# Optimization experiments

Measured on AMD Instinct MI355X. Metric: run time of the kernel, lower is better.

Reference implementation:

```python
import jax, jax.numpy as jnp
import numpy as np

D = 64      # in_feats
OUT = 64    # out_feats
MEM = 4     # mem_size
NREL = 8    # num_rels
N = 20000   # num nodes
E = 50000   # num edges
FF = 16     # dim_feedforward (hardcoded in module)
NH = 4      # nhead (hardcoded)
EPS = 1e-5  # LayerNorm eps (torch default)


def _ln(x, w, b):
    m = x.mean(-1, keepdims=True)
    v = ((x - m) ** 2).mean(-1, keepdims=True)
    return (x - m) * jax.lax.rsqrt(v + EPS) * w + b


def _enc(x, Wqkv, bqkv, Wo, bo, W1, b1, W2, b2, ln1w, ln1b, ln2w, ln2b):
    # torch TransformerEncoderLayer, batch_first, post-norm, eval mode, no padding mask (all-zero mask)
    B, S, d = x.shape
    dh = d // NH
    qkv = x @ Wqkv.T + bqkv
    q, k, v = jnp.split(qkv, 3, axis=-1)
    q = q.reshape(B, S, NH, dh)
    k = k.reshape(B, S, NH, dh)
    v = v.reshape(B, S, NH, dh)
    att = jax.nn.softmax(jnp.einsum('bqhd,bkhd->bhqk', q, k) / jnp.sqrt(jnp.float32(dh)), axis=-1)
    o = jnp.einsum('bhqk,bkhd->bqhd', att, v).reshape(B, S, d) @ Wo.T + bo
    x = _ln(x + o, ln1w, ln1b)
    ff = jax.nn.relu(x @ W1.T + b1) @ W2.T + b2
    return _ln(x + ff, ln2w, ln2b)


def setup_inputs() -> dict:
    key = jax.random.key(0)
    ks = jax.random.split(key, 16)
    s = 0.05
    inp = {
        'feat': jax.random.normal(ks[0], (N, D), jnp.float32),
        'src_idx': jax.random.randint(ks[1], (E,), 0, N),
        'dst_idx': jax.random.randint(ks[2], (E,), 0, N),
        'etype': jax.random.randint(ks[3], (E,), 0, NREL),
        'Wqkv': jax.random.normal(ks[4], (3 * D, D), jnp.float32) * s,
        'bqkv': jnp.zeros((3 * D,), jnp.float32),
        'Wo': jax.random.normal(ks[5], (D, D), jnp.float32) * s,
        'bo': jnp.zeros((D,), jnp.float32),
        'W1': jax.random.normal(ks[6], (FF, D), jnp.float32) * s,
        'b1': jnp.zeros((FF,), jnp.float32),
        'W2': jax.random.normal(ks[7], (D, FF), jnp.float32) * s,
        'b2': jnp.zeros((D,), jnp.float32),
        'ln1w': jnp.ones((D,), jnp.float32),
        'ln1b': jnp.zeros((D,), jnp.float32),
        'ln2w': jnp.ones((D,), jnp.float32),
        'ln2b': jnp.zeros((D,), jnp.float32),
        'Wc': jax.random.normal(ks[8], (MEM, D), jnp.float32) * s,
        'bc': jnp.zeros((MEM,), jnp.float32),
        'CLS': jax.random.normal(ks[9], (MEM, D), jnp.float32),
        'SEP': jax.random.normal(ks[10], (D,), jnp.float32),
        'Wm': jax.random.normal(ks[11], (OUT * D, D), jnp.float32) * s,
        'h_bias': jnp.zeros((OUT,), jnp.float32),
    }
    return inp


def reference(feat, src_idx, dst_idx, etype, Wqkv, bqkv, Wo, bo, W1, b1, W2, b2,
              ln1w, ln1b, ln2w, ln2b, Wc, bc, CLS, SEP, Wm, h_bias):
    enc_args = (Wqkv, bqkv, Wo, bo, W1, b1, W2, b2, ln1w, ln1b, ln2w, ln2b)

    def cls_pass(s_, d_):
        # run the shared encoder MEM times with a different CLS token; the math
        # is identical for every relation type, so no per-etype partition needed
        B = s_.shape[0]
        outs = []
        mem = jnp.zeros((B, D), s_.dtype)
        for i in range(MEM):
            cls = jnp.broadcast_to(CLS[i], (B, D))[:, None, :]
            sep = jnp.broadcast_to(SEP, (B, D))[:, None, :]
            seq = jnp.concatenate([cls, s_[:, None, :], sep, d_[:, None, :]], axis=1)  # [B,4,D]
            t = _enc(seq, *enc_args)[:, 0, :]
            outs.append(t)
            mem = mem + t
        return mem, jnp.stack(outs)  # [B,D], [MEM,B,D]

    src = feat[src_idx]  # [E,D]
    dst = feat[dst_idx]
    mem_emb, tmps = cls_pass(src, dst)
    cat_all = tmps @ Wc.T + bc               # [MEM,E,MEM]
    w = (mem_emb @ Wm.T).reshape(E, OUT, D)  # per-edge hypernetwork weight
    msg = jnp.einsum('eoi,ei->eo', w, src)   # [E,OUT]

    # dgl fn.mean aggregation over destination nodes (0 for isolated nodes)
    cnt = jax.ops.segment_sum(jnp.ones((E,), msg.dtype), dst_idx, num_segments=N)
    agg = jax.ops.segment_sum(msg, dst_idx, num_segments=N)
    node_rep = jnp.where(cnt[:, None] > 0, agg / jnp.maximum(cnt, 1.0)[:, None], 0.0)
    node_rep = node_rep + h_bias

    # self loop (same hypernetwork path over every node)
    mem_s, _ = cls_pass(feat, feat)
    hs = (mem_s @ Wm.T).reshape(N, OUT, D)
    node_rep = node_rep + jnp.einsum('noi,ni->no', hs, feat)

    # reconstruct torch concat order of category/label: outer loop etype, inner loop mem idx
    et = etype.astype(jnp.int32)
    counts = jax.ops.segment_sum(jnp.ones((E,), jnp.int32), etype, num_segments=NREL)
    start = jnp.concatenate([jnp.zeros((1,), jnp.int32), jnp.cumsum(counts)[:-1].astype(jnp.int32)])
    order = jnp.argsort(etype, stable=True)
    rank = jnp.zeros((E,), jnp.int32).at[order].set(jnp.arange(E, dtype=jnp.int32) - start[et[order]])
    base = start[et] * MEM + rank                                            # [E]
    pos = base[None, :] + jnp.arange(MEM, dtype=jnp.int32)[:, None] * counts[et][None, :]  # [MEM,E]
    category = jnp.zeros((MEM * E, MEM), cat_all.dtype).at[pos.reshape(-1)].set(cat_all.reshape(-1, MEM))
    label = jnp.zeros((MEM * E,), jnp.int32).at[pos.reshape(-1)].set(
        jnp.repeat(jnp.arange(MEM, dtype=jnp.int32), E))
    return node_rep, label, category
```

## Files before the change

### kernel.cpp

```cpp
#include <hip/hip_runtime.h>
#include <hip/hip_bf16.h>

typedef float f32x4_t __attribute__((ext_vector_type(4)));
typedef short bf16x8_t __attribute__((ext_vector_type(8)));

#define MFMA(a, b, c) __builtin_amdgcn_mfma_f32_16x16x32_bf16(a, b, c, 0, 0, 0)

#define C_Q0   0
#define C_S00  256
#define C_S02  272
#define C_VCLS 288
#define C_VSEP 544

__device__ __forceinline__ short f2bf(float x) {
    return (short)__builtin_bit_cast(unsigned short, __float2bfloat16(x));
}
__device__ __forceinline__ float bf2f(short s) {
    return __builtin_bit_cast(float, ((unsigned)(unsigned short)s) << 16);
}
__device__ __forceinline__ float head_sum16(float v) {
#pragma unroll
    for (int off = 1; off < 16; off <<= 1) v += __shfl_xor(v, off, 64);
    return v;
}

__global__ void k_prep(const float* __restrict__ Wo, const float* __restrict__ Wqkv,
                       const float* __restrict__ W1, const float* __restrict__ W2,
                       const float* __restrict__ Wm, const float* __restrict__ Wc,
                       const float* __restrict__ bqkv,
                       const float* __restrict__ CLS, const float* __restrict__ SEP,
                       const int* __restrict__ etype, const int* __restrict__ dst,
                       short* __restrict__ Bpack, short* __restrict__ WoP,
                       short* __restrict__ WkvP, short* __restrict__ W1P,
                       short* __restrict__ W2P, short* __restrict__ WcP,
                       float* __restrict__ consts,
                       int* __restrict__ hist, int* __restrict__ cnt, int E)
{
    int bx = blockIdx.x;
    if (bx < 136) {
        int tid = bx * 256 + threadIdx.x;
        short tmp[8];
        if (tid < 32768) {
            int u = tid, lane = u & 63, nt = (u >> 6) & 3, kstep = u >> 8;
            int o = nt * 16 + (lane & 15);
            int kb = kstep * 32 + (lane >> 4) * 8;
#pragma unroll
            for (int t = 0; t < 8; t++) { int k = kb + t; tmp[t] = f2bf(Wm[(o * 64 + (k >> 6)) * 64 + (k & 63)]); }
            *(bf16x8_t*)&Bpack[(size_t)u * 8] = *(bf16x8_t*)tmp;
        } else if (tid < 33280) {
            int u = tid - 32768, lane = u & 63, nt = (u >> 6) & 3, kstep = u >> 8;
            int o = nt * 16 + (lane & 15), kb = kstep * 32 + (lane >> 4) * 8;
#pragma unroll
            for (int t = 0; t < 8; t++) tmp[t] = f2bf(Wo[o * 64 + kb + t]);
            *(bf16x8_t*)&WoP[(size_t)u * 8] = *(bf16x8_t*)tmp;
        } else if (tid < 34304) {
            int u = tid - 33280, lane = u & 63, nt = (u >> 6) & 7, kstep = u >> 9;
            int col = nt * 16 + (lane & 15), kb = kstep * 32 + (lane >> 4) * 8;
            int row = 64 + col;
#pragma unroll
            for (int t = 0; t < 8; t++) tmp[t] = f2bf(Wqkv[row * 64 + kb + t]);
            *(bf16x8_t*)&WkvP[(size_t)u * 8] = *(bf16x8_t*)tmp;
        } else if (tid < 34432) {
            int u = tid - 34304, lane = u & 63, kstep = u >> 6;
            int f = lane & 15, kb = kstep * 32 + (lane >> 4) * 8;
#pragma unroll
            for (int t = 0; t < 8; t++) tmp[t] = f2bf(W1[f * 64 + kb + t]);
            *(bf16x8_t*)&W1P[(size_t)u * 8] = *(bf16x8_t*)tmp;
        } else if (tid < 34688) {
            int u = tid - 34432, lane = u & 63, nt = u >> 6;
            int o = nt * 16 + (lane & 15), kb = (lane >> 4) * 8;
#pragma unroll
            for (int t = 0; t < 8; t++) { int k = kb + t; tmp[t] = (k < 16) ? f2bf(W2[o * 16 + k]) : (short)0; }
            *(bf16x8_t*)&W2P[(size_t)u * 8] = *(bf16x8_t*)tmp;
        } else if (tid < 34816) {
            int u = tid - 34688, lane = u & 63, kstep = u >> 6;
            int m = lane & 15, kb = kstep * 32 + (lane >> 4) * 8;
#pragma unroll
            for (int t = 0; t < 8; t++) tmp[t] = (m < 4) ? f2bf(Wc[m * 64 + kb + t]) : (short)0;
            *(bf16x8_t*)&WcP[(size_t)u * 8] = *(bf16x8_t*)tmp;
        }
    } else if (bx == 136) {
        if (threadIdx.x < 64) {
            int lane = threadIdx.x;
            float ksep = bqkv[64 + lane], vsep = bqkv[128 + lane];
            for (int c = 0; c < 64; c++) {
                float sc = SEP[c];
                ksep += Wqkv[(64 + lane) * 64 + c] * sc;
                vsep += Wqkv[(128 + lane) * 64 + c] * sc;
            }
            consts[C_VSEP + lane] = vsep;
            for (int i = 0; i < 4; i++) {
                float q0 = bqkv[lane], kcls = bqkv[64 + lane], vcls = bqkv[128 + lane];
                for (int c = 0; c < 64; c++) {
                    float cc = CLS[i * 64 + c];
                    q0   += Wqkv[lane * 64 + c] * cc;
                    kcls += Wqkv[(64 + lane) * 64 + c] * cc;
                    vcls += Wqkv[(128 + lane) * 64 + c] * cc;
                }
                consts[C_Q0 + i * 64 + lane] = q0;
                consts[C_VCLS + i * 64 + lane] = vcls;
                float p00 = head_sum16(q0 * kcls) * 0.25f;
                float p02 = head_sum16(q0 * ksep) * 0.25f;
                if ((lane & 15) == 0) {
                    consts[C_S00 + i * 4 + (lane >> 4)] = p00;
                    consts[C_S02 + i * 4 + (lane >> 4)] = p02;
                }
            }
        }
    } else {
        __shared__ int h[8];
        int chunk = bx - 137;
        int tid = threadIdx.x;
        if (tid < 8) h[tid] = 0;
        __syncthreads();
        int e = chunk * 256 + tid;
        if (e < E) {
            atomicAdd(&h[etype[e]], 1);
            atomicAdd(&cnt[dst[e]], 1);
        }
        __syncthreads();
        if (tid < 8) hist[chunk * 8 + tid] = h[tid];
    }
}

__global__ void k_scan(const int* __restrict__ hist, int* __restrict__ chunkoff,
                       int* __restrict__ startg, int* __restrict__ countsg, int nch,
                       const float* __restrict__ consts, const float* __restrict__ Wqkv,
                       const float* __restrict__ bqkv,
                       short* __restrict__ WqkP, float* __restrict__ bqk)
{
    int lane = threadIdx.x;
    int g = lane & 7, seg = lane >> 3;
    int per = (nch + 7) / 8;
    int c0 = seg * per, c1 = c0 + per; if (c1 > nch) c1 = nch;
    int sum = 0;
    for (int c = c0; c < c1; c++) sum += hist[c * 8 + g];
    int pre = 0, tot = 0;
#pragma unroll
    for (int s2 = 0; s2 < 8; s2++) {
        int v = __shfl(sum, s2 * 8 + g, 64);
        tot += v;
        if (s2 < seg) pre += v;
    }
    int run = pre;
    for (int c = c0; c < c1; c++) { chunkoff[c * 8 + g] = run; run += hist[c * 8 + g]; }
    if (seg == 0) {
        countsg[g] = tot;
        int sg = 0;
#pragma unroll
        for (int g2 = 0; g2 < 8; g2++) { int v = __shfl(tot, g2, 64); if (g2 < g) sg += v; }
        startg[g] = sg;
    }

    int ih = lane & 15, ii = ih & 3, hh = ih >> 2;
    int lh8 = (lane >> 4) * 8;
    short tmp[8];
#pragma unroll
    for (int kstep = 0; kstep < 2; kstep++) {
#pragma unroll
        for (int t = 0; t < 8; t++) {
            int k = kstep * 32 + lh8 + t;
            float s = 0.f;
            for (int u = 0; u < 16; u++)
                s += consts[C_Q0 + ii * 64 + hh * 16 + u] * Wqkv[(64 + hh * 16 + u) * 64 + k];
            tmp[t] = f2bf(0.25f * s);
        }
        *(bf16x8_t*)&WqkP[(size_t)(kstep * 64 + lane) * 8] = *(bf16x8_t*)tmp;
    }
    if (lane < 16) {
        float s = 0.f;
        for (int u = 0; u < 16; u++)
            s += consts[C_Q0 + ii * 64 + hh * 16 + u] * bqkv[64 + hh * 16 + u];
        bqk[lane] = 0.25f * s;
    }
}

__global__ __launch_bounds__(256) void k_kv(const float* __restrict__ feat,
        const short* __restrict__ WkvP, const short* __restrict__ WqkP,
        const float* __restrict__ bqkv, const float* __restrict__ bqk,
        float* __restrict__ vnode, float* __restrict__ qs, int N)
{
    __shared__ __align__(16) short sA[64 * 72];
    int tid = threadIdx.x, lane = tid & 63, w = tid >> 6;
    int l15 = lane & 15, lh = lane >> 4;
    int base = blockIdx.x * 64;
#pragma unroll
    for (int rr = 0; rr < 16; rr++) {
        int row = w * 16 + rr;
        int n = base + row; n = n < N ? n : N - 1;
        sA[row * 72 + lane] = f2bf(feat[(size_t)n * 64 + lane]);
    }
    __syncthreads();
    const bf16x8_t* bp = (const bf16x8_t*)WkvP;
    bf16x8_t bv0 = bp[(0 * 8 + 4 + w) * 64 + lane];
    bf16x8_t bv1 = bp[(1 * 8 + 4 + w) * 64 + lane];
    bf16x8_t bq0 = ((const bf16x8_t*)WqkP)[lane];
    bf16x8_t bq1 = ((const bf16x8_t*)WqkP)[64 + lane];
    int kof = lh * 8;
    int col = w * 16 + l15;
    float biasv = bqkv[128 + col];
    float bqv = bqk[l15];
#pragma unroll
    for (int rt = 0; rt < 4; rt++) {
        bf16x8_t a0 = *(const bf16x8_t*)&sA[(rt * 16 + l15) * 72 + kof];
        bf16x8_t a1 = *(const bf16x8_t*)&sA[(rt * 16 + l15) * 72 + 32 + kof];
        f32x4_t av = {0.f, 0.f, 0.f, 0.f};
        av = MFMA(a0, bv0, av); av = MFMA(a1, bv1, av);
#pragma unroll
        for (int r = 0; r < 4; r++) {
            int n = base + rt * 16 + lh * 4 + r;
            if (n < N) vnode[(size_t)n * 64 + col] = av[r] + biasv;
        }
        if (w == 0) {
            f32x4_t aq = {0.f, 0.f, 0.f, 0.f};
            aq = MFMA(a0, bq0, aq); aq = MFMA(a1, bq1, aq);
#pragma unroll
            for (int r = 0; r < 4; r++) {
                int n = base + rt * 16 + lh * 4 + r;
                if (n < N) qs[(size_t)n * 16 + l15] = aq[r] + bqv;
            }
        }
    }
}

struct EncW {
    const float* consts; const float* CLS; const float* bo;
    const float* b1; const float* b2;
    const float* ln1w; const float* ln1b; const float* ln2w; const float* ln2b;
    const short* WoP; const short* W1P; const short* W2P; const short* WcP;
    const float* bc;
};

__global__ __launch_bounds__(256) void k_enc(const int* __restrict__ src_idx,
        const int* __restrict__ dst_idx,
        const float* __restrict__ vnode, const float* __restrict__ qs, EncW W,
        float* __restrict__ mem_out, float* __restrict__ cat_out, int E, int M)
{
    __shared__ __align__(16) short sA[64 * 72];
    __shared__ __align__(16) short sF[64 * 40];
    int tid = threadIdx.x, lane = tid & 63, w = tid >> 6;
    int l15 = lane & 15, lh = lane >> 4;
    int base = blockIdx.x * 16;

#pragma unroll
    for (int z = 0; z < 4; z++) {
        int zz = z * 64 + lane;
        sF[(w * 16 + (zz >> 4)) * 40 + 16 + (zz & 15)] = 0;
    }

    float attc[4], esum0[4];
#pragma unroll
    for (int i = 0; i < 4; i++) {
        float e0 = __expf(W.consts[C_S00 + i * 4 + lh]);
        float e2 = __expf(W.consts[C_S02 + i * 4 + lh]);
        attc[i]  = e0 * W.consts[C_VCLS + i * 64 + lane] + e2 * W.consts[C_VSEP + lane];
        esum0[i] = e0 + e2;
    }

#pragma unroll
    for (int el = 0; el < 4; el++) {
        int eloc = w * 4 + el;
        int ge = base + eloc; int gc = ge < M ? ge : M - 1;
        int s, d;
        if (gc < E) { s = src_idx[gc]; d = dst_idx[gc]; }
        else        { s = gc - E; d = s; }
        float vs_ = vnode[(size_t)s * 64 + lane];
        float vd  = vnode[(size_t)d * 64 + lane];
        float4 qh_s = *(const float4*)&qs[(size_t)s * 16 + lh * 4];
        float4 qh_d = *(const float4*)&qs[(size_t)d * 16 + lh * 4];
        float qsv[4] = {qh_s.x, qh_s.y, qh_s.z, qh_s.w};
        float qdv[4] = {qh_d.x, qh_d.y, qh_d.z, qh_d.w};
#pragma unroll
        for (int i = 0; i < 4; i++) {
            float e1 = __expf(qsv[i]), e3 = __expf(qdv[i]);
            float inv = 1.0f / (esum0[i] + e1 + e3);
            float att = (attc[i] + e1 * vs_ + e3 * vd) * inv;
            sA[(eloc * 4 + i) * 72 + lane] = f2bf(att);
        }
    }

    int arow = (w * 16 + l15) * 72;
    int kof = lh * 8;

    const bf16x8_t* bpo = (const bf16x8_t*)W.WoP;
    f32x4_t ac0 = {0.f,0.f,0.f,0.f}, ac1 = ac0, ac2 = ac0, ac3 = ac0;
#pragma unroll
    for (int kstep = 0; kstep < 2; kstep++) {
        bf16x8_t a = *(const bf16x8_t*)&sA[arow + kstep * 32 + kof];
        ac0 = MFMA(a, bpo[(kstep * 4 + 0) * 64 + lane], ac0);
        ac1 = MFMA(a, bpo[(kstep * 4 + 1) * 64 + lane], ac1);
        ac2 = MFMA(a, bpo[(kstep * 4 + 2) * 64 + lane], ac2);
        ac3 = MFMA(a, bpo[(kstep * 4 + 3) * 64 + lane], ac3);
    }

    float x[4][4], y[4][4];
#pragma unroll
    for (int r = 0; r < 4; r++) { x[0][r] = ac0[r]; x[1][r] = ac1[r]; x[2][r] = ac2[r]; x[3][r] = ac3[r]; }
    float lw1[4], lb1[4];
#pragma unroll
    for (int nt = 0; nt < 4; nt++) {
        float b = W.bo[nt * 16 + l15];
        lw1[nt] = W.ln1w[nt * 16 + l15]; lb1[nt] = W.ln1b[nt * 16 + l15];
#pragma unroll
        for (int r = 0; r < 4; r++) x[nt][r] += b + W.CLS[r * 64 + nt * 16 + l15];
    }
#pragma unroll
    for (int r = 0; r < 4; r++) {
        float sm = head_sum16(x[0][r] + x[1][r] + x[2][r] + x[3][r]);
        float mu = sm * 0.015625f;
        float vv = 0.f;
#pragma unroll
        for (int nt = 0; nt < 4; nt++) { float dd = x[nt][r] - mu; vv = fmaf(dd, dd, vv); }
        vv = head_sum16(vv);
        float rs = rsqrtf(vv * 0.015625f + 1e-5f);
#pragma unroll
        for (int nt = 0; nt < 4; nt++) y[nt][r] = (x[nt][r] - mu) * rs * lw1[nt] + lb1[nt];
    }
#pragma unroll
    for (int nt = 0; nt < 4; nt++)
#pragma unroll
        for (int r = 0; r < 4; r++)
            sA[(w * 16 + lh * 4 + r) * 72 + nt * 16 + l15] = f2bf(y[nt][r]);

    const bf16x8_t* bp1 = (const bf16x8_t*)W.W1P;
    f32x4_t fa = {0.f,0.f,0.f,0.f};
#pragma unroll
    for (int kstep = 0; kstep < 2; kstep++) {
        bf16x8_t a = *(const bf16x8_t*)&sA[arow + kstep * 32 + kof];
        fa = MFMA(a, bp1[kstep * 64 + lane], fa);
    }
    float b1v = W.b1[l15];
#pragma unroll
    for (int r = 0; r < 4; r++)
        sF[(w * 16 + lh * 4 + r) * 40 + l15] = f2bf(fmaxf(fa[r] + b1v, 0.f));

    const bf16x8_t* bp2 = (const bf16x8_t*)W.W2P;
    bf16x8_t af = *(const bf16x8_t*)&sF[(w * 16 + l15) * 40 + kof];
    f32x4_t z0 = {0.f,0.f,0.f,0.f}, z1 = z0, z2 = z0, z3 = z0;
    z0 = MFMA(af, bp2[0 * 64 + lane], z0);
    z1 = MFMA(af, bp2[1 * 64 + lane], z1);
    z2 = MFMA(af, bp2[2 * 64 + lane], z2);
    z3 = MFMA(af, bp2[3 * 64 + lane], z3);

    float t[4][4];
#pragma unroll
    for (int r = 0; r < 4; r++) { x[0][r] = z0[r]; x[1][r] = z1[r]; x[2][r] = z2[r]; x[3][r] = z3[r]; }
    float lw2[4], lb2[4];
#pragma unroll
    for (int nt = 0; nt < 4; nt++) {
        float b = W.b2[nt * 16 + l15];
        lw2[nt] = W.ln2w[nt * 16 + l15]; lb2[nt] = W.ln2b[nt * 16 + l15];
#pragma unroll
        for (int r = 0; r < 4; r++) x[nt][r] += b + y[nt][r];
    }
#pragma unroll
    for (int r = 0; r < 4; r++) {
        float sm = head_sum16(x[0][r] + x[1][r] + x[2][r] + x[3][r]);
        float mu = sm * 0.015625f;
        float vv = 0.f;
#pragma unroll
        for (int nt = 0; nt < 4; nt++) { float dd = x[nt][r] - mu; vv = fmaf(dd, dd, vv); }
        vv = head_sum16(vv);
        float rs = rsqrtf(vv * 0.015625f + 1e-5f);
#pragma unroll
        for (int nt = 0; nt < 4; nt++) t[nt][r] = (x[nt][r] - mu) * rs * lw2[nt] + lb2[nt];
    }

    int eloc = w * 4 + lh, ge = base + eloc;

    if (base < E) {
#pragma unroll
        for (int nt = 0; nt < 4; nt++)
#pragma unroll
            for (int r = 0; r < 4; r++)
                sA[(w * 16 + lh * 4 + r) * 72 + nt * 16 + l15] = f2bf(t[nt][r]);
        const bf16x8_t* bpc = (const bf16x8_t*)W.WcP;
        f32x4_t ca = {0.f,0.f,0.f,0.f};
#pragma unroll
        for (int kstep = 0; kstep < 2; kstep++) {
            bf16x8_t a = *(const bf16x8_t*)&sA[arow + kstep * 32 + kof];
            ca = MFMA(a, bpc[kstep * 64 + lane], ca);
        }
        if (l15 < 4 && ge < E) {
            float bcv = W.bc[l15];
#pragma unroll
            for (int r = 0; r < 4; r++)
                cat_out[((size_t)r * E + ge) * 4 + l15] = ca[r] + bcv;
        }
    }

    if (ge < M) {
#pragma unroll
        for (int nt = 0; nt < 4; nt++)
            mem_out[(size_t)ge * 64 + nt * 16 + l15] = t[nt][0] + t[nt][1] + t[nt][2] + t[nt][3];
    }
}

__global__ __launch_bounds__(256, 3) void k_hyper(
        const float* __restrict__ feat, const int* __restrict__ src_idx,
        const int* __restrict__ dst_idx, const float* __restrict__ memall,
        const short* __restrict__ Bpack,
        float* __restrict__ agg, float* __restrict__ selfm, int E, int M)
{
    __shared__ short xsT[64 * 132];
    __shared__ __align__(16) short sB[2][8192];
    int tid = threadIdx.x, lane = tid & 63, w = tid >> 6;
    int l15 = lane & 15, lh = lane >> 4, koff = lh * 8;
    int base = blockIdx.x * 128;

    const bf16x8_t* bp = (const bf16x8_t*)Bpack;

    auto stage = [&](int c, int buf) {
#pragma unroll
        for (int jj = 0; jj < 4; ++jj) {
            int j = w * 4 + jj;
            int il_ic = j >> 3, q = j & 7;
            const short* src = (const short*)(bp + (size_t)(c * 2 + il_ic) * 512
                                              + (q >> 2) * 256 + (q & 3) * 64 + lane);
            short* dst = &sB[buf][j * 512];
            __builtin_amdgcn_global_load_lds(
                (const __attribute__((address_space(1))) void*)src,
                (__attribute__((address_space(3))) void*)dst, 16, 0, 0);
        }
    };

    stage(0, 0);

    for (int rr = 0; rr < 32; ++rr) {
        int row = w * 32 + rr, gr = base + row;
        float xv = 0.f;
        if (gr < M) {
            int xi = gr < E ? src_idx[gr] : gr - E;
            xv = feat[(size_t)xi * 64 + lane];
        }
        xsT[lane * 132 + row] = f2bf(xv);
    }

    bf16x8_t am[2][2];
#pragma unroll
    for (int tt = 0; tt < 2; ++tt) {
        int gr = base + w * 32 + tt * 16 + l15;
        const float* mp = memall + (size_t)(gr < M ? gr : 0) * 64 + koff;
#pragma unroll
        for (int kk = 0; kk < 2; ++kk)
#pragma unroll
            for (int t = 0; t < 8; ++t)
                am[tt][kk][t] = f2bf(mp[kk * 32 + t]);
    }

    f32x4_t out[2][4];
#pragma unroll
    for (int tt = 0; tt < 2; ++tt)
#pragma unroll
        for (int nt = 0; nt < 4; ++nt) out[tt][nt] = (f32x4_t){0.f, 0.f, 0.f, 0.f};
    const f32x4_t ZERO = {0.f, 0.f, 0.f, 0.f};

    int xrow0 = w * 32 + lh * 4;

    int cur = 0;
    for (int c = 0; c < 32; ++c) {
        if (c + 1 < 32) {
            stage(c + 1, cur ^ 1);
            asm volatile("s_waitcnt vmcnt(4)" ::: "memory");
        } else {
            asm volatile("s_waitcnt vmcnt(0)" ::: "memory");
        }
        __builtin_amdgcn_s_barrier();
#pragma unroll
        for (int ic = 0; ic < 2; ++ic) {
            int i = c * 2 + ic;
            unsigned long long xw0 = *(const unsigned long long*)&xsT[i * 132 + xrow0];
            unsigned long long xw1 = *(const unsigned long long*)&xsT[i * 132 + xrow0 + 16];
            float x0[4], x1[4];
            {
                unsigned lo0 = (unsigned)xw0, hi0 = (unsigned)(xw0 >> 32);
                unsigned lo1 = (unsigned)xw1, hi1 = (unsigned)(xw1 >> 32);
                x0[0] = __builtin_bit_cast(float, lo0 << 16);
                x0[1] = __builtin_bit_cast(float, lo0 & 0xffff0000u);
                x0[2] = __builtin_bit_cast(float, hi0 << 16);
                x0[3] = __builtin_bit_cast(float, hi0 & 0xffff0000u);
                x1[0] = __builtin_bit_cast(float, lo1 << 16);
                x1[1] = __builtin_bit_cast(float, lo1 & 0xffff0000u);
                x1[2] = __builtin_bit_cast(float, hi1 << 16);
                x1[3] = __builtin_bit_cast(float, hi1 & 0xffff0000u);
            }
            const bf16x8_t* bfr = (const bf16x8_t*)&sB[cur][ic * 4096];
            f32x4_t P0[4], P1[4];
            __builtin_amdgcn_s_setprio(1);
#pragma unroll
            for (int nt = 0; nt < 4; ++nt) {
                bf16x8_t B0 = bfr[nt * 64 + lane];
                bf16x8_t B1 = bfr[(4 + nt) * 64 + lane];
                P0[nt] = MFMA(am[0][0], B0, ZERO);
                P1[nt] = MFMA(am[1][0], B0, ZERO);
                P0[nt] = MFMA(am[0][1], B1, P0[nt]);
                P1[nt] = MFMA(am[1][1], B1, P1[nt]);
            }
            __builtin_amdgcn_s_setprio(0);
#pragma unroll
            for (int nt = 0; nt < 4; ++nt)
#pragma unroll
                for (int r = 0; r < 4; ++r) {
                    out[0][nt][r] = fmaf(x0[r], P0[nt][r], out[0][nt][r]);
                    out[1][nt][r] = fmaf(x1[r], P1[nt][r], out[1][nt][r]);
                }
        }
        __builtin_amdgcn_s_barrier();
        cur ^= 1;
    }

#pragma unroll
    for (int tt = 0; tt < 2; ++tt) {
        int orow = w * 32 + tt * 16 + lh * 4;
        int di[4];
#pragma unroll
        for (int r = 0; r < 4; ++r) {
            int grow = base + orow + r;
            di[r] = (grow < E) ? dst_idx[grow] : 0;
        }
#pragma unroll
        for (int nt = 0; nt < 4; ++nt) {
            int o = nt * 16 + l15;
#pragma unroll
            for (int r = 0; r < 4; ++r) {
                int grow = base + orow + r;
                if (grow < M) {
                    float v = out[tt][nt][r];
                    if (grow < E) atomicAdd(&agg[(size_t)di[r] * 64 + o], v);
                    else selfm[(size_t)(grow - E) * 64 + o] = v;
                }
            }
        }
    }
}

__global__ __launch_bounds__(256) void k_finsc(
        const float* __restrict__ agg, const int* __restrict__ cnt,
        const float* __restrict__ selfm, const float* __restrict__ h_bias,
        float* __restrict__ outp, int N,
        const int* __restrict__ etype, const float* __restrict__ cat_all,
        const int* __restrict__ chunkoff, const int* __restrict__ startg,
        const int* __restrict__ countsg,
        float* __restrict__ out_label, float* __restrict__ out_cat, int E, int FB)
{
    if ((int)blockIdx.x < FB) {
        int t = blockIdx.x * 256 + threadIdx.x;
        if (t < N * 64) {
            int n = t >> 6, o = t & 63;
            int c = cnt[n];
            float av = (c > 0) ? agg[t] / (float)c : 0.f;
            outp[t] = av + h_bias[o] + selfm[t];
        }
    } else {
        __shared__ int wc[4][8];
        int tid = threadIdx.x, lane = tid & 63, w = tid >> 6;
        int chunk = blockIdx.x - FB;
        int e = chunk * 256 + w * 64 + lane;
        int et = (e < E) ? etype[e] : -1;
        unsigned long long mk[8];
#pragma unroll
        for (int g = 0; g < 8; g++) mk[g] = __ballot(et == g);
        if (lane < 8) wc[w][lane] = (int)__popcll(mk[lane]);
        __syncthreads();
        if (et >= 0) {
            unsigned long long lt = (1ull << lane) - 1ull;
            int myr = chunkoff[chunk * 8 + et] + (int)__popcll(mk[et] & lt);
#pragma unroll
            for (int w2 = 0; w2 < 4; w2++) if (w2 < w) myr += wc[w2][et];
            int sg = startg[et], cg = countsg[et];
            size_t pbase = (size_t)sg * 4 + myr;
#pragma unroll
            for (int i = 0; i < 4; i++) {
                size_t pos = pbase + (size_t)i * cg;
                out_label[pos] = (float)i;
                const float* ca = &cat_all[((size_t)i * E + e) * 4];
                float4 cv = {ca[0], ca[1], ca[2], ca[3]};
                *(float4*)&out_cat[pos * 4] = cv;
            }
        }
    }
}

extern "C" void kernel_launch(void* const* d_in, const int* in_sizes, int n_in,
                              void* d_out, int out_size, void* d_ws, size_t ws_size,
                              hipStream_t stream)
{
    const float* feat    = (const float*)d_in[0];
    const int*   src_idx = (const int*)d_in[1];
    const int*   dst_idx = (const int*)d_in[2];
    const int*   etype   = (const int*)d_in[3];
    const float* Wqkv    = (const float*)d_in[4];
    const float* bqkv    = (const float*)d_in[5];
    const float* Wo      = (const float*)d_in[6];
    const float* bo      = (const float*)d_in[7];
    const float* W1      = (const float*)d_in[8];
    const float* b1      = (const float*)d_in[9];
    const float* W2      = (const float*)d_in[10];
    const float* b2      = (const float*)d_in[11];
    const float* ln1w    = (const float*)d_in[12];
    const float* ln1b    = (const float*)d_in[13];
    const float* ln2w    = (const float*)d_in[14];
    const float* ln2b    = (const float*)d_in[15];
    const float* Wc      = (const float*)d_in[16];
    const float* bc      = (const float*)d_in[17];
    const float* CLS     = (const float*)d_in[18];
    const float* SEP     = (const float*)d_in[19];
    const float* Wm      = (const float*)d_in[20];
    const float* h_bias  = (const float*)d_in[21];

    const int N = in_sizes[0] / 64;
    const int E = in_sizes[1];
    const int M = E + N;
    const int NCH = (E + 255) / 256;
    const int FB = (N * 64 + 255) / 256;

    float* ws = (float*)d_ws;
    size_t off = 0;
    auto alloc = [&](size_t n) { float* p = ws + off; off += (n + 63) & ~(size_t)63; return p; };
    float* qs      = alloc((size_t)N * 16);
    float* vnode   = alloc((size_t)N * 64);
    float* mem_all = alloc((size_t)M * 64);
    float* cat_all = alloc((size_t)E * 16);
    float* agg     = alloc((size_t)N * 64 + N);
    int*   cnt     = (int*)(agg + (size_t)N * 64);
    float* selfm   = alloc((size_t)N * 64);
    float* consts  = alloc(1024);
    short* Bpack   = (short*)alloc(131072);
    short* WoP     = (short*)alloc(2048);
    short* WkvP    = (short*)alloc(4096);
    short* W1P     = (short*)alloc(512);
    short* W2P     = (short*)alloc(1024);
    short* WcP     = (short*)alloc(512);
    short* WqkP    = (short*)alloc(512);
    float* bqk     = alloc(64);
    int*   hist    = (int*)alloc(NCH * 8);
    int*   chunkoff= (int*)alloc(NCH * 8);
    int*   startg  = (int*)alloc(8);
    int*   countsg = (int*)alloc(8);

    float* out_node  = (float*)d_out;
    float* out_label = out_node + (size_t)N * 64;
    float* out_cat   = out_label + (size_t)4 * E;

    hipMemsetAsync(agg, 0, ((size_t)N * 64 + N) * sizeof(float), stream);

    k_prep<<<137 + NCH, 256, 0, stream>>>(Wo, Wqkv, W1, W2, Wm, Wc, bqkv, CLS, SEP,
                                          etype, dst_idx, Bpack, WoP, WkvP, W1P, W2P, WcP,
                                          consts, hist, cnt, E);
    k_scan<<<1, 64, 0, stream>>>(hist, chunkoff, startg, countsg, NCH,
                                 consts, Wqkv, bqkv, WqkP, bqk);

    k_kv<<<(N + 63) / 64, 256, 0, stream>>>(feat, WkvP, WqkP, bqkv, bqk, vnode, qs, N);

    EncW W{consts, CLS, bo, b1, b2, ln1w, ln1b, ln2w, ln2b, WoP, W1P, W2P, WcP, bc};

    k_enc<<<(M + 15) / 16, 256, 0, stream>>>(src_idx, dst_idx, vnode, qs, W,
                                             mem_all, cat_all, E, M);

    k_hyper<<<(M + 127) / 128, 256, 0, stream>>>(feat, src_idx, dst_idx, mem_all, Bpack,
                                                 agg, selfm, E, M);

    k_finsc<<<FB + NCH, 256, 0, stream>>>(agg, cnt, selfm, h_bias, out_node, N,
                                          etype, cat_all, chunkoff, startg, countsg,
                                          out_label, out_cat, E, FB);
}
```

Measured before the change: 147.2 us.

## Eliminate k_scan launch by folding its work into k_prep and k_kv

Removes the single-block k_scan kernel. The WqkP/bqk weight-folding moves into a new dedicated block of k_prep, now parallelized over 256 threads with shared memory, and the etype histogram scan runs as an extra block appended to k_kv. This saves one serial launch and a tiny low-occupancy kernel on the critical path. Separately, the double-buffered loop in k_hyper is rearranged to wait for all loads, issue one barrier, then prefetch the next stage, dropping the trailing barrier but waiting fully each iteration.

```diff
diff --git a/kernel.cpp b/kernel.cpp
--- a/kernel.cpp
+++ b/kernel.cpp
@@ -34,6 +34,7 @@
                        short* __restrict__ WkvP, short* __restrict__ W1P,
                        short* __restrict__ W2P, short* __restrict__ WcP,
                        float* __restrict__ consts,
+                       short* __restrict__ WqkP, float* __restrict__ bqk,
                        int* __restrict__ hist, int* __restrict__ cnt, int E)
 {
     int bx = blockIdx.x;
@@ -107,9 +108,48 @@
                 }
             }
         }
+    } else if (bx == 137) {
+        __shared__ float q0s[4][64];
+        __shared__ float wqk[16][64];
+        int tid = threadIdx.x;
+        {
+            int i = tid >> 6, c = tid & 63;
+            float q0 = bqkv[c];
+            for (int c2 = 0; c2 < 64; c2++)
+                q0 += Wqkv[c * 64 + c2] * CLS[i * 64 + c2];
+            q0s[i][c] = q0;
+        }
+        __syncthreads();
+#pragma unroll
+        for (int q = 0; q < 4; q++) {
+            int idx = tid * 4 + q;
+            int ih = idx >> 6, k = idx & 63;
+            int ii = ih & 3, hh = ih >> 2;
+            float s = 0.f;
+#pragma unroll
+            for (int u = 0; u < 16; u++)
+                s += q0s[ii][hh * 16 + u] * Wqkv[(64 + hh * 16 + u) * 64 + k];
+            wqk[ih][k] = 0.25f * s;
+        }
+        __syncthreads();
+        if (tid < 128) {
+            int kstep = tid >> 6, lane = tid & 63;
+            short tmp[8];
+#pragma unroll
+            for (int t = 0; t < 8; t++)
+                tmp[t] = f2bf(wqk[lane & 15][kstep * 32 + (lane >> 4) * 8 + t]);
+            *(bf16x8_t*)&WqkP[(size_t)(kstep * 64 + lane) * 8] = *(bf16x8_t*)tmp;
+        } else if (tid < 144) {
+            int ihh = tid - 128, ii = ihh & 3, hh = ihh >> 2;
+            float s = 0.f;
+#pragma unroll
+            for (int u = 0; u < 16; u++)
+                s += q0s[ii][hh * 16 + u] * bqkv[64 + hh * 16 + u];
+            bqk[ihh] = 0.25f * s;
+        }
     } else {
         __shared__ int h[8];
-        int chunk = bx - 137;
+        int chunk = bx - 138;
         int tid = threadIdx.x;
         if (tid < 8) h[tid] = 0;
         __syncthreads();
@@ -123,63 +163,40 @@
     }
 }
 
-__global__ void k_scan(const int* __restrict__ hist, int* __restrict__ chunkoff,
-                       int* __restrict__ startg, int* __restrict__ countsg, int nch,
-                       const float* __restrict__ consts, const float* __restrict__ Wqkv,
-                       const float* __restrict__ bqkv,
-                       short* __restrict__ WqkP, float* __restrict__ bqk)
-{
-    int lane = threadIdx.x;
-    int g = lane & 7, seg = lane >> 3;
-    int per = (nch + 7) / 8;
-    int c0 = seg * per, c1 = c0 + per; if (c1 > nch) c1 = nch;
-    int sum = 0;
-    for (int c = c0; c < c1; c++) sum += hist[c * 8 + g];
-    int pre = 0, tot = 0;
-#pragma unroll
-    for (int s2 = 0; s2 < 8; s2++) {
-        int v = __shfl(sum, s2 * 8 + g, 64);
-        tot += v;
-        if (s2 < seg) pre += v;
-    }
-    int run = pre;
-    for (int c = c0; c < c1; c++) { chunkoff[c * 8 + g] = run; run += hist[c * 8 + g]; }
-    if (seg == 0) {
-        countsg[g] = tot;
-        int sg = 0;
-#pragma unroll
-        for (int g2 = 0; g2 < 8; g2++) { int v = __shfl(tot, g2, 64); if (g2 < g) sg += v; }
-        startg[g] = sg;
-    }
-
-    int ih = lane & 15, ii = ih & 3, hh = ih >> 2;
-    int lh8 = (lane >> 4) * 8;
-    short tmp[8];
-#pragma unroll
-    for (int kstep = 0; kstep < 2; kstep++) {
-#pragma unroll
-        for (int t = 0; t < 8; t++) {
-            int k = kstep * 32 + lh8 + t;
-            float s = 0.f;
-            for (int u = 0; u < 16; u++)
-                s += consts[C_Q0 + ii * 64 + hh * 16 + u] * Wqkv[(64 + hh * 16 + u) * 64 + k];
-            tmp[t] = f2bf(0.25f * s);
-        }
-        *(bf16x8_t*)&WqkP[(size_t)(kstep * 64 + lane) * 8] = *(bf16x8_t*)tmp;
-    }
-    if (lane < 16) {
-        float s = 0.f;
-        for (int u = 0; u < 16; u++)
-            s += consts[C_Q0 + ii * 64 + hh * 16 + u] * bqkv[64 + hh * 16 + u];
-        bqk[lane] = 0.25f * s;
-    }
-}
-
 __global__ __launch_bounds__(256) void k_kv(const float* __restrict__ feat,
         const short* __restrict__ WkvP, const short* __restrict__ WqkP,
         const float* __restrict__ bqkv, const float* __restrict__ bqk,
-        float* __restrict__ vnode, float* __restrict__ qs, int N)
+        float* __restrict__ vnode, float* __restrict__ qs, int N,
+        const int* __restrict__ hist, int* __restrict__ chunkoff,
+        int* __restrict__ startg, int* __restrict__ countsg, int nch, int KB)
 {
+    if ((int)blockIdx.x == KB) {
+        if (threadIdx.x < 64) {
+            int lane = threadIdx.x;
+            int g = lane & 7, seg = lane >> 3;
+            int per = (nch + 7) / 8;
+            int c0 = seg * per, c1 = c0 + per; if (c1 > nch) c1 = nch;
+            int sum = 0;
+            for (int c = c0; c < c1; c++) sum += hist[c * 8 + g];
+            int pre = 0, tot = 0;
+#pragma unroll
+            for (int s2 = 0; s2 < 8; s2++) {
+                int v = __shfl(sum, s2 * 8 + g, 64);
+                tot += v;
+                if (s2 < seg) pre += v;
+            }
+            int run = pre;
+            for (int c = c0; c < c1; c++) { chunkoff[c * 8 + g] = run; run += hist[c * 8 + g]; }
+            if (seg == 0) {
+                countsg[g] = tot;
+                int sg = 0;
+#pragma unroll
+                for (int g2 = 0; g2 < 8; g2++) { int v = __shfl(tot, g2, 64); if (g2 < g) sg += v; }
+                startg[g] = sg;
+            }
+        }
+        return;
+    }
     __shared__ __align__(16) short sA[64 * 72];
     int tid = threadIdx.x, lane = tid & 63, w = tid >> 6;
     int l15 = lane & 15, lh = lane >> 4;
@@ -459,13 +476,9 @@
 
     int cur = 0;
     for (int c = 0; c < 32; ++c) {
-        if (c + 1 < 32) {
-            stage(c + 1, cur ^ 1);
-            asm volatile("s_waitcnt vmcnt(4)" ::: "memory");
-        } else {
-            asm volatile("s_waitcnt vmcnt(0)" ::: "memory");
-        }
+        asm volatile("s_waitcnt vmcnt(0)" ::: "memory");
         __builtin_amdgcn_s_barrier();
+        if (c + 1 < 32) stage(c + 1, cur ^ 1);
 #pragma unroll
         for (int ic = 0; ic < 2; ++ic) {
             int i = c * 2 + ic;
@@ -505,7 +518,6 @@
                     out[1][nt][r] = fmaf(x1[r], P1[nt][r], out[1][nt][r]);
                 }
         }
-        __builtin_amdgcn_s_barrier();
         cur ^= 1;
     }
 
@@ -613,6 +625,7 @@
     const int M = E + N;
     const int NCH = (E + 255) / 256;
     const int FB = (N * 64 + 255) / 256;
+    const int KB = (N + 63) / 64;
 
     float* ws = (float*)d_ws;
     size_t off = 0;
@@ -644,13 +657,12 @@
 
     hipMemsetAsync(agg, 0, ((size_t)N * 64 + N) * sizeof(float), stream);
 
-    k_prep<<<137 + NCH, 256, 0, stream>>>(Wo, Wqkv, W1, W2, Wm, Wc, bqkv, CLS, SEP,
+    k_prep<<<138 + NCH, 256, 0, stream>>>(Wo, Wqkv, W1, W2, Wm, Wc, bqkv, CLS, SEP,
                                           etype, dst_idx, Bpack, WoP, WkvP, W1P, W2P, WcP,
-                                          consts, hist, cnt, E);
-    k_scan<<<1, 64, 0, stream>>>(hist, chunkoff, startg, countsg, NCH,
-                                 consts, Wqkv, bqkv, WqkP, bqk);
-
-    k_kv<<<(N + 63) / 64, 256, 0, stream>>>(feat, WkvP, WqkP, bqkv, bqk, vnode, qs, N);
+                                          consts, WqkP, bqk, hist, cnt, E);
+
+    k_kv<<<KB + 1, 256, 0, stream>>>(feat, WkvP, WqkP, bqkv, bqk, vnode, qs, N,
+                                     hist, chunkoff, startg, countsg, NCH, KB);
 
     EncW W{consts, CLS, bo, b1, b2, ln1w, ln1b, ln2w, ln2b, WoP, W1P, W2P, WcP, bc};
 
```

Result: faster. 138.8 us, median of 3 (-5.7%).
